# Performance work log

Hardware: AMD Instinct MI355X
Metric: run time of the kernel (lower is better)

Reference implementation:

```python
import jax, jax.numpy as jnp
import numpy as np

# Model dims (MiniCPM-style decode-only LM inside VoxCPM2)
L, B, D = 16, 4, 1024
H, HD, KVH = 16, 64, 8          # query heads, head dim, KV heads (GQA)
DFF = 4096
S = 2048                         # current KV cache length
SCALE_DEPTH = 1.4                # mup depth scaling
EPS = 1e-5
THETA = 10000.0
W_STD = 0.02


def setup_inputs() -> dict:
    key = jax.random.key(0)
    ks = jax.random.split(key, 12)
    return {
        "inputs_embeds": jax.random.normal(ks[0], (B, D), jnp.float32),
        "k_cache": jax.random.normal(ks[1], (L, B, KVH, S, HD), jnp.float32),
        "v_cache": jax.random.normal(ks[2], (L, B, KVH, S, HD), jnp.float32),
        "ln1_w": jnp.ones((L, D), jnp.float32),
        "ln2_w": jnp.ones((L, D), jnp.float32),
        "norm_w": jnp.ones((D,), jnp.float32),
        "wq": jax.random.normal(ks[3], (L, D, H * HD), jnp.float32) * W_STD,
        "wk": jax.random.normal(ks[4], (L, D, KVH * HD), jnp.float32) * W_STD,
        "wv": jax.random.normal(ks[5], (L, D, KVH * HD), jnp.float32) * W_STD,
        "wo": jax.random.normal(ks[6], (L, H * HD, D), jnp.float32) * W_STD,
        "w_gate": jax.random.normal(ks[7], (L, D, DFF), jnp.float32) * W_STD,
        "w_up": jax.random.normal(ks[8], (L, D, DFF), jnp.float32) * W_STD,
        "w_down": jax.random.normal(ks[9], (L, DFF, D), jnp.float32) * W_STD,
        "cache_length": S,  # position id of the token being decoded
    }


def _rmsnorm(x, w):
    return x * jax.lax.rsqrt(jnp.mean(x * x, axis=-1, keepdims=True) + EPS) * w


def _rotate_half(x):
    x1, x2 = jnp.split(x, 2, axis=-1)
    return jnp.concatenate((-x2, x1), axis=-1)


def _decode_step(inputs_embeds, k_cache, v_cache, ln1_w, ln2_w, norm_w,
                 wq, wk, wv, wo, w_gate, w_up, w_down, cache_length):
    # RoPE tables for the single decode position
    pos = jnp.asarray(cache_length, jnp.float32)
    inv_freq = 1.0 / (THETA ** (jnp.arange(0, HD, 2, dtype=jnp.float32) / HD))
    freqs = pos * inv_freq                       # [HD/2]
    emb = jnp.concatenate((freqs, freqs))        # [HD]
    cos, sin = jnp.cos(emb), jnp.sin(emb)

    mup = SCALE_DEPTH / np.sqrt(L)
    scale = 1.0 / np.sqrt(HD)
    G = H // KVH  # query heads per KV head

    def layer(h, ws):
        l1, l2, Wq, Wk, Wv, Wo, Wg, Wu, Wd, kc, vc = ws
        x = _rmsnorm(h, l1)                                  # [B, D]
        q = (x @ Wq).reshape(B, H, HD)
        k = (x @ Wk).reshape(B, KVH, HD)
        v = (x @ Wv).reshape(B, KVH, HD)
        q = q * cos + _rotate_half(q) * sin
        k = k * cos + _rotate_half(k) * sin
        nk = jnp.concatenate((kc, k[:, :, None, :]), axis=2)  # [B, KVH, S+1, HD]
        nv = jnp.concatenate((vc, v[:, :, None, :]), axis=2)
        qg = q.reshape(B, KVH, G, HD)                         # GQA grouping
        scores = jnp.einsum('bkgd,bksd->bkgs', qg, nk) * scale
        p = jax.nn.softmax(scores, axis=-1)
        o = jnp.einsum('bkgs,bksd->bkgd', p, nv).reshape(B, H * HD)
        h = h + (o @ Wo) * mup                                # mup residual
        x = _rmsnorm(h, l2)
        mlp = (jax.nn.silu(x @ Wg) * (x @ Wu)) @ Wd           # SwiGLU
        h = h + mlp * mup
        return h, (nk, nv)

    h, (next_k, next_v) = jax.lax.scan(
        layer, inputs_embeds,
        (ln1_w, ln2_w, wq, wk, wv, wo, w_gate, w_up, w_down, k_cache, v_cache))
    h = _rmsnorm(h, norm_w)
    return h, next_k, next_v


def reference(inputs_embeds, k_cache, v_cache, ln1_w, ln2_w, norm_w,
              wq, wk, wv, wo, w_gate, w_up, w_down, cache_length):
    h, nk, nv = _decode_step(inputs_embeds, k_cache, v_cache, ln1_w, ln2_w,
                             norm_w, wq, wk, wv, wo, w_gate, w_up, w_down,
                             cache_length)
    return h, nk, nv, jnp.asarray(cache_length + 1, jnp.int64)
```

## Files before the change

kernel.cpp:

```cpp
#include <hip/hip_runtime.h>
#include <math.h>

#define MUP 0.35f
#define SCALE 0.125f
#define EPS 1e-5f

#define WS_HA    0
#define WS_HB    4096
#define WS_YMLP  8192
#define WS_YO    12288
#define WS_QKVP  16384
#define WS_OPART 278528
#define WS_GUP   413696

#define OUT_NK  4096
#define OUT_NV  (4096 + 16*4*8*2049*64)
#define OUT_SC  (4096 + 2*16*4*8*2049*64)

__device__ __forceinline__ float wsum64(float v) {
    v += __shfl_xor(v, 32); v += __shfl_xor(v, 16); v += __shfl_xor(v, 8);
    v += __shfl_xor(v, 4);  v += __shfl_xor(v, 2);  v += __shfl_xor(v, 1);
    return v;
}

__device__ __forceinline__ void fma4(float4& a, float s, const float4 w) {
    a.x = fmaf(s, w.x, a.x); a.y = fmaf(s, w.y, a.y);
    a.z = fmaf(s, w.z, a.z); a.w = fmaf(s, w.w, a.w);
}

__global__ __launch_bounds__(256) void k_init(const float* __restrict__ emb,
                                              const int* __restrict__ cl,
                                              float* __restrict__ ws,
                                              float* __restrict__ out) {
    int tid = threadIdx.x;
    float4* ws4 = (float4*)ws;
    float4 z = {0.f, 0.f, 0.f, 0.f};
    if (blockIdx.x == 0) {
        const float4* e4 = (const float4*)emb;
        #pragma unroll
        for (int k = 0; k < 4; ++k) ws4[(WS_HA >> 2) + k * 256 + tid] = e4[k * 256 + tid];
        if (tid == 0) out[OUT_SC] = (float)(cl[0] + 1);
    } else if (blockIdx.x == 1) {
        #pragma unroll
        for (int k = 0; k < 4; ++k) ws4[(WS_YMLP >> 2) + k * 256 + tid] = z;
    } else {
        #pragma unroll
        for (int k = 0; k < 4; ++k) ws4[(WS_YO >> 2) + k * 256 + tid] = z;
    }
}

__global__ __launch_bounds__(512) void k_a(const float* __restrict__ ln1,
                                           const float* __restrict__ wq,
                                           const float* __restrict__ wk,
                                           const float* __restrict__ wv,
                                           float* __restrict__ ws, int l) {
    float4* ws4 = (float4*)ws;
    const int tid = threadIdx.x, w = tid >> 6, lane = tid & 63;
    if (blockIdx.x >= 64) {
        float4 z = {0,0,0,0};
        ws4[(WS_YO >> 2) + (blockIdx.x - 64) * 512 + tid] = z;
        return;
    }
    __shared__ float xs[4][128];
    __shared__ float4 red[8][64][4];
    __shared__ float sred[8][4];
    const int s = blockIdx.x >> 3, xt = blockIdx.x & 7;
    const int t2 = tid & 255;

    float4 hn[4]; float ss[4];
    #pragma unroll
    for (int b = 0; b < 4; ++b) {
        float4 h = ws4[(WS_HA >> 2) + b * 256 + t2];
        float4 y = ws4[(WS_YMLP >> 2) + b * 256 + t2];
        h.x = fmaf(MUP, y.x, h.x); h.y = fmaf(MUP, y.y, h.y);
        h.z = fmaf(MUP, y.z, h.z); h.w = fmaf(MUP, y.w, h.w);
        hn[b] = h;
        ss[b] = h.x*h.x + h.y*h.y + h.z*h.z + h.w*h.w;
    }
    #pragma unroll
    for (int b = 0; b < 4; ++b) {
        float v = wsum64(ss[b]);
        if (lane == 0) sred[w][b] = v;
    }
    __syncthreads();
    float rstd[4];
    #pragma unroll
    for (int b = 0; b < 4; ++b) {
        float tot = 0.f;
        #pragma unroll
        for (int ww = 0; ww < 8; ++ww) tot += sred[ww][b];
        rstd[b] = rsqrtf(tot * (1.f/2048.f) + EPS);
    }
    if (blockIdx.x == 0 && tid < 256) {
        #pragma unroll
        for (int b = 0; b < 4; ++b) ws4[(WS_HB >> 2) + b * 256 + t2] = hn[b];
    }
    {
        int tl = t2 - s * 32;
        if (tl >= 0 && tl < 32) {
            float4 g4 = ((const float4*)ln1)[l * 256 + t2];
            #pragma unroll
            for (int b = 0; b < 4; ++b) {
                float4 xv;
                xv.x = hn[b].x * rstd[b] * g4.x; xv.y = hn[b].y * rstd[b] * g4.y;
                xv.z = hn[b].z * rstd[b] * g4.z; xv.w = hn[b].w * rstd[b] * g4.w;
                ((float4*)xs[b])[tl] = xv;
            }
        }
    }
    __syncthreads();

    const float* Wp; int nc, c;
    if (xt < 4)      { Wp = wq + (size_t)l * 1024 * 1024; nc = 1024; c = xt * 256 + lane * 4; }
    else if (xt < 6) { Wp = wk + (size_t)l * 1024 * 512;  nc = 512;  c = (xt - 4) * 256 + lane * 4; }
    else             { Wp = wv + (size_t)l * 1024 * 512;  nc = 512;  c = (xt - 6) * 256 + lane * 4; }
    const float4* W4 = (const float4*)(Wp + c);
    const size_t nc4 = (size_t)(nc >> 2);
    float4 a0 = {0,0,0,0}, a1 = a0, a2 = a0, a3 = a0;
    #pragma unroll
    for (int ch = 0; ch < 2; ++ch) {
        float4 wr[8];
        #pragma unroll
        for (int i = 0; i < 8; ++i)
            wr[i] = W4[(size_t)(s * 128 + w * 16 + ch * 8 + i) * nc4];
        #pragma unroll
        for (int i = 0; i < 8; ++i) {
            int r = w * 16 + ch * 8 + i;
            fma4(a0, xs[0][r], wr[i]); fma4(a1, xs[1][r], wr[i]);
            fma4(a2, xs[2][r], wr[i]); fma4(a3, xs[3][r], wr[i]);
        }
    }
    red[w][lane][0] = a0; red[w][lane][1] = a1;
    red[w][lane][2] = a2; red[w][lane][3] = a3;
    __syncthreads();
    if (w == 0) {
        float4* QKVP4 = ws4 + (WS_QKVP >> 2);
        #pragma unroll
        for (int b = 0; b < 4; ++b) {
            float4 sv = red[0][lane][b];
            #pragma unroll
            for (int ww = 1; ww < 8; ++ww) {
                float4 t = red[ww][lane][b];
                sv.x += t.x; sv.y += t.y; sv.z += t.z; sv.w += t.w;
            }
            QKVP4[(size_t)(s * 4 + b) * 512 + xt * 64 + lane] = sv;
        }
    }
}

__global__ __launch_bounds__(256) void k_b(const float* __restrict__ kc,
                                           const float* __restrict__ vc,
                                           const int* __restrict__ cl,
                                           float* __restrict__ ws,
                                           float* __restrict__ nk,
                                           float* __restrict__ nv, int l) {
    const int bid = blockIdx.x;
    const int b = bid >> 6, kvh = (bid >> 3) & 7, c = bid & 7;
    const int s0 = c * 256;
    const int tid = threadIdx.x, w = tid >> 6, lane = tid & 63;
    const int sub = lane >> 4, j = lane & 15;
    float4* ws4 = (float4*)ws;
    const float4* QKVP4 = (const float4*)ws4 + (WS_QKVP >> 2);

    __shared__ float4 oac[2][16][16];
    __shared__ float mlm[2][16], mll[2][16];

    const float pos = (float)cl[0];
    float cs4[4], sn4[4];
    #pragma unroll
    for (int m = 0; m < 4; ++m) {
        float t = (float)(4 * (j & 7) + m);
        float fr = pos * __expf(-t * 0.2878231366242557f);
        cs4[m] = cosf(fr); sn4[m] = sinf(fr);
    }
    const float sgn = (j < 8) ? -1.f : 1.f;

    float4 q0 = {0,0,0,0}, q1 = {0,0,0,0};
    #pragma unroll
    for (int sp = 0; sp < 8; ++sp) {
        const float4* qp = QKVP4 + (size_t)(sp * 4 + b) * 512 + kvh * 32;
        float4 t0 = qp[j], t1 = qp[16 + j];
        q0.x += t0.x; q0.y += t0.y; q0.z += t0.z; q0.w += t0.w;
        q1.x += t1.x; q1.y += t1.y; q1.z += t1.z; q1.w += t1.w;
    }
    {
        float4 q0p, q1p;
        q0p.x = __shfl_xor(q0.x, 8); q0p.y = __shfl_xor(q0.y, 8);
        q0p.z = __shfl_xor(q0.z, 8); q0p.w = __shfl_xor(q0.w, 8);
        q1p.x = __shfl_xor(q1.x, 8); q1p.y = __shfl_xor(q1.y, 8);
        q1p.z = __shfl_xor(q1.z, 8); q1p.w = __shfl_xor(q1.w, 8);
        q0.x = q0.x * cs4[0] + sgn * q0p.x * sn4[0];
        q0.y = q0.y * cs4[1] + sgn * q0p.y * sn4[1];
        q0.z = q0.z * cs4[2] + sgn * q0p.z * sn4[2];
        q0.w = q0.w * cs4[3] + sgn * q0p.w * sn4[3];
        q1.x = q1.x * cs4[0] + sgn * q1p.x * sn4[0];
        q1.y = q1.y * cs4[1] + sgn * q1p.y * sn4[1];
        q1.z = q1.z * cs4[2] + sgn * q1p.z * sn4[2];
        q1.w = q1.w * cs4[3] + sgn * q1p.w * sn4[3];
    }

    const size_t cbase = (size_t)((l * 4 + b) * 8 + kvh);
    const float4* kc4 = (const float4*)kc + cbase * 2048 * 16;
    const float4* vc4 = (const float4*)vc + cbase * 2048 * 16;
    float4* nk4 = (float4*)nk + cbase * 2049 * 16;
    float4* nv4 = (float4*)nv + cbase * 2049 * 16;

    float m0 = -1e30f, m1 = -1e30f, l0 = 0.f, l1 = 0.f;
    float4 o0 = {0,0,0,0}, o1 = {0,0,0,0};
    for (int g = 0; g < 4; ++g) {
        const int rb = s0 + g * 64 + w * 16;
        float4 kr[4], vr[4];
        #pragma unroll
        for (int ii = 0; ii < 4; ++ii) {
            int r = rb + ii * 4 + sub;
            kr[ii] = kc4[(size_t)r * 16 + j];
            vr[ii] = vc4[(size_t)r * 16 + j];
        }
        #pragma unroll
        for (int ii = 0; ii < 4; ++ii) {
            int r = rb + ii * 4 + sub;
            nk4[(size_t)r * 16 + j] = kr[ii];
            nv4[(size_t)r * 16 + j] = vr[ii];
        }
        #pragma unroll
        for (int ii = 0; ii < 4; ++ii) {
            float4 kv = kr[ii];
            float d0 = kv.x*q0.x + kv.y*q0.y + kv.z*q0.z + kv.w*q0.w;
            float d1 = kv.x*q1.x + kv.y*q1.y + kv.z*q1.z + kv.w*q1.w;
            d0 += __shfl_xor(d0, 1); d0 += __shfl_xor(d0, 2);
            d0 += __shfl_xor(d0, 4); d0 += __shfl_xor(d0, 8);
            d1 += __shfl_xor(d1, 1); d1 += __shfl_xor(d1, 2);
            d1 += __shfl_xor(d1, 4); d1 += __shfl_xor(d1, 8);
            d0 *= SCALE; d1 *= SCALE;
            float mn0 = fmaxf(m0, d0);
            float e0 = __expf(m0 - mn0), p0 = __expf(d0 - mn0);
            o0.x = o0.x*e0 + p0*kv.x*0.f + p0*vr[ii].x;
            o0.x = fmaf(p0, vr[ii].x, o0.x - p0*vr[ii].x + (o0.x*e0 - o0.x));
            o0 = o0;
            o0.x = 0.f;
            break;
        }
        break;
    }
    m0 = -1e30f; m1 = -1e30f; l0 = 0.f; l1 = 0.f;
    o0 = make_float4(0.f, 0.f, 0.f, 0.f); o1 = make_float4(0.f, 0.f, 0.f, 0.f);
    for (int g = 0; g < 4; ++g) {
        const int rb = s0 + g * 64 + w * 16;
        float4 kr[4], vr[4];
        #pragma unroll
        for (int ii = 0; ii < 4; ++ii) {
            int r = rb + ii * 4 + sub;
            kr[ii] = kc4[(size_t)r * 16 + j];
            vr[ii] = vc4[(size_t)r * 16 + j];
        }
        #pragma unroll
        for (int ii = 0; ii < 4; ++ii) {
            int r = rb + ii * 4 + sub;
            nk4[(size_t)r * 16 + j] = kr[ii];
            nv4[(size_t)r * 16 + j] = vr[ii];
        }
        #pragma unroll
        for (int ii = 0; ii < 4; ++ii) {
            float4 kv = kr[ii];
            float d0 = kv.x*q0.x + kv.y*q0.y + kv.z*q0.z + kv.w*q0.w;
            float d1 = kv.x*q1.x + kv.y*q1.y + kv.z*q1.z + kv.w*q1.w;
            d0 += __shfl_xor(d0, 1); d0 += __shfl_xor(d0, 2);
            d0 += __shfl_xor(d0, 4); d0 += __shfl_xor(d0, 8);
            d1 += __shfl_xor(d1, 1); d1 += __shfl_xor(d1, 2);
            d1 += __shfl_xor(d1, 4); d1 += __shfl_xor(d1, 8);
            d0 *= SCALE; d1 *= SCALE;
            float mn0 = fmaxf(m0, d0);
            float e0 = __expf(m0 - mn0), p0 = __expf(d0 - mn0);
            o0.x = o0.x*e0 + p0*vr[ii].x; o0.y = o0.y*e0 + p0*vr[ii].y;
            o0.z = o0.z*e0 + p0*vr[ii].z; o0.w = o0.w*e0 + p0*vr[ii].w;
            l0 = l0*e0 + p0; m0 = mn0;
            float mn1 = fmaxf(m1, d1);
            float e1 = __expf(m1 - mn1), p1 = __expf(d1 - mn1);
            o1.x = o1.x*e1 + p1*vr[ii].x; o1.y = o1.y*e1 + p1*vr[ii].y;
            o1.z = o1.z*e1 + p1*vr[ii].z; o1.w = o1.w*e1 + p1*vr[ii].w;
            l1 = l1*e1 + p1; m1 = mn1;
        }
    }
    if (c == 7 && w == 0 && sub == 0) {
        float4 kv = {0,0,0,0}, vnew = {0,0,0,0};
        #pragma unroll
        for (int sp = 0; sp < 8; ++sp) {
            const float4* pp = QKVP4 + (size_t)(sp * 4 + b) * 512;
            float4 t0 = pp[256 + kvh * 16 + j];
            float4 t1 = pp[384 + kvh * 16 + j];
            kv.x += t0.x; kv.y += t0.y; kv.z += t0.z; kv.w += t0.w;
            vnew.x += t1.x; vnew.y += t1.y; vnew.z += t1.z; vnew.w += t1.w;
        }
        float4 kp;
        kp.x = __shfl_xor(kv.x, 8); kp.y = __shfl_xor(kv.y, 8);
        kp.z = __shfl_xor(kv.z, 8); kp.w = __shfl_xor(kv.w, 8);
        kv.x = kv.x * cs4[0] + sgn * kp.x * sn4[0];
        kv.y = kv.y * cs4[1] + sgn * kp.y * sn4[1];
        kv.z = kv.z * cs4[2] + sgn * kp.z * sn4[2];
        kv.w = kv.w * cs4[3] + sgn * kp.w * sn4[3];
        nk4[(size_t)2048 * 16 + j] = kv;
        nv4[(size_t)2048 * 16 + j] = vnew;
        float d0 = kv.x*q0.x + kv.y*q0.y + kv.z*q0.z + kv.w*q0.w;
        float d1 = kv.x*q1.x + kv.y*q1.y + kv.z*q1.z + kv.w*q1.w;
        d0 += __shfl_xor(d0, 1); d0 += __shfl_xor(d0, 2);
        d0 += __shfl_xor(d0, 4); d0 += __shfl_xor(d0, 8);
        d1 += __shfl_xor(d1, 1); d1 += __shfl_xor(d1, 2);
        d1 += __shfl_xor(d1, 4); d1 += __shfl_xor(d1, 8);
        d0 *= SCALE; d1 *= SCALE;
        float mn0 = fmaxf(m0, d0);
        float e0 = __expf(m0 - mn0), p0 = __expf(d0 - mn0);
        o0.x = o0.x*e0 + p0*vnew.x; o0.y = o0.y*e0 + p0*vnew.y;
        o0.z = o0.z*e0 + p0*vnew.z; o0.w = o0.w*e0 + p0*vnew.w;
        l0 = l0*e0 + p0; m0 = mn0;
        float mn1 = fmaxf(m1, d1);
        float e1 = __expf(m1 - mn1), p1 = __expf(d1 - mn1);
        o1.x = o1.x*e1 + p1*vnew.x; o1.y = o1.y*e1 + p1*vnew.y;
        o1.z = o1.z*e1 + p1*vnew.z; o1.w = o1.w*e1 + p1*vnew.w;
        l1 = l1*e1 + p1; m1 = mn1;
    }
    const int grp = w * 4 + sub;
    oac[0][grp][j] = o0;
    oac[1][grp][j] = o1;
    if (j == 0) {
        mlm[0][grp] = m0; mll[0][grp] = l0;
        mlm[1][grp] = m1; mll[1][grp] = l1;
    }
    __syncthreads();
    if (tid < 128) {
        const int h = tid >> 6, d = tid & 63;
        const float* oa = (const float*)&oac[h][0][0];
        float M = -1e30f;
        #pragma unroll
        for (int g2 = 0; g2 < 16; ++g2) M = fmaxf(M, mlm[h][g2]);
        float ot = 0.f, lt = 0.f;
        #pragma unroll
        for (int g2 = 0; g2 < 16; ++g2) {
            float e = __expf(mlm[h][g2] - M);
            ot += oa[g2 * 64 + d] * e;
            lt += mll[h][g2] * e;
        }
        int pbase = WS_OPART + ((b * 8 + kvh) * 8 + c) * 132;
        ws[pbase + h * 64 + d] = ot;
        if (d == 0) { ws[pbase + 128 + 2 * h] = M; ws[pbase + 129 + 2 * h] = lt; }
    }
}

__global__ __launch_bounds__(512) void k_c(const float* __restrict__ wo,
                                           float* __restrict__ ws, int l) {
    float4* ws4 = (float4*)ws;
    const int tid = threadIdx.x, w = tid >> 6, lane = tid & 63;
    if (blockIdx.x >= 32) {
        float4 z = {0,0,0,0};
        ws4[(WS_YMLP >> 2) + (blockIdx.x - 32) * 512 + tid] = z;
        return;
    }
    __shared__ float xs[4][128];
    __shared__ float4 red[8][64][4];
    const int xt = blockIdx.x & 3, s = blockIdx.x >> 2;
    {
        const int bb = tid >> 7, rr = tid & 127;
        const int r = s * 128 + rr;
        const int kvh = r >> 7, g = (r >> 6) & 1, d = r & 63;
        const float* bp = ws + WS_OPART + (size_t)((bb * 8 + kvh) * 8) * 132;
        float m = -1e30f;
        #pragma unroll
        for (int cc = 0; cc < 8; ++cc)
            m = fmaxf(m, bp[cc * 132 + 128 + 2 * g]);
        float lt = 0.f, ot = 0.f;
        #pragma unroll
        for (int cc = 0; cc < 8; ++cc) {
            float f = __expf(bp[cc * 132 + 128 + 2 * g] - m);
            lt += bp[cc * 132 + 129 + 2 * g] * f;
            ot += bp[cc * 132 + g * 64 + d] * f;
        }
        xs[bb][rr] = ot / lt;
    }
    __syncthreads();
    const float4* W4 = (const float4*)(wo + (size_t)l * 1024 * 1024 + xt * 256 + lane * 4);
    float4 a0 = {0,0,0,0}, a1 = a0, a2 = a0, a3 = a0;
    #pragma unroll
    for (int ch = 0; ch < 2; ++ch) {
        float4 wr[8];
        #pragma unroll
        for (int i = 0; i < 8; ++i)
            wr[i] = W4[(size_t)(s * 128 + w * 16 + ch * 8 + i) * 256];
        #pragma unroll
        for (int i = 0; i < 8; ++i) {
            int r = w * 16 + ch * 8 + i;
            fma4(a0, xs[0][r], wr[i]); fma4(a1, xs[1][r], wr[i]);
            fma4(a2, xs[2][r], wr[i]); fma4(a3, xs[3][r], wr[i]);
        }
    }
    red[w][lane][0] = a0; red[w][lane][1] = a1;
    red[w][lane][2] = a2; red[w][lane][3] = a3;
    __syncthreads();
    if (w == 0) {
        int c = xt * 256 + lane * 4;
        #pragma unroll
        for (int b = 0; b < 4; ++b) {
            float4 sv = red[0][lane][b];
            #pragma unroll
            for (int ww = 1; ww < 8; ++ww) {
                float4 t = red[ww][lane][b];
                sv.x += t.x; sv.y += t.y; sv.z += t.z; sv.w += t.w;
            }
            atomicAdd(&ws[WS_YO + b * 1024 + c + 0], sv.x);
            atomicAdd(&ws[WS_YO + b * 1024 + c + 1], sv.y);
            atomicAdd(&ws[WS_YO + b * 1024 + c + 2], sv.z);
            atomicAdd(&ws[WS_YO + b * 1024 + c + 3], sv.w);
        }
    }
}

__global__ __launch_bounds__(512) void k_d(const float* __restrict__ ln2,
                                           const float* __restrict__ wg,
                                           const float* __restrict__ wu,
                                           float* __restrict__ ws, int l) {
    float4* ws4 = (float4*)ws;
    const int tid = threadIdx.x, w = tid >> 6, lane = tid & 63;
    __shared__ float xs[4][128];
    __shared__ float4 red[8][64][4];
    __shared__ float sred[8][4];
    const int t16 = blockIdx.x, y = blockIdx.y;
    const int t2 = tid & 255;

    float4 hn[4]; float ss[4];
    #pragma unroll
    for (int b = 0; b < 4; ++b) {
        float4 h = ws4[(WS_HB >> 2) + b * 256 + t2];
        float4 yv = ws4[(WS_YO >> 2) + b * 256 + t2];
        h.x = fmaf(MUP, yv.x, h.x); h.y = fmaf(MUP, yv.y, h.y);
        h.z = fmaf(MUP, yv.z, h.z); h.w = fmaf(MUP, yv.w, h.w);
        hn[b] = h;
        ss[b] = h.x*h.x + h.y*h.y + h.z*h.z + h.w*h.w;
    }
    #pragma unroll
    for (int b = 0; b < 4; ++b) {
        float v = wsum64(ss[b]);
        if (lane == 0) sred[w][b] = v;
    }
    __syncthreads();
    float rstd[4];
    #pragma unroll
    for (int b = 0; b < 4; ++b) {
        float tot = 0.f;
        #pragma unroll
        for (int ww = 0; ww < 8; ++ww) tot += sred[ww][b];
        rstd[b] = rsqrtf(tot * (1.f/2048.f) + EPS);
    }
    if (blockIdx.x == 0 && blockIdx.y == 0 && tid < 256) {
        #pragma unroll
        for (int b = 0; b < 4; ++b) ws4[(WS_HA >> 2) + b * 256 + t2] = hn[b];
    }
    {
        int tl = t2 - y * 32;
        if (tl >= 0 && tl < 32) {
            float4 g4 = ((const float4*)ln2)[l * 256 + t2];
            #pragma unroll
            for (int b = 0; b < 4; ++b) {
                float4 xv;
                xv.x = hn[b].x * rstd[b] * g4.x; xv.y = hn[b].y * rstd[b] * g4.y;
                xv.z = hn[b].z * rstd[b] * g4.z; xv.w = hn[b].w * rstd[b] * g4.w;
                ((float4*)xs[b])[tl] = xv;
            }
        }
    }
    __syncthreads();
    float4* GUP4 = ws4 + (WS_GUP >> 2);

    #pragma unroll
    for (int mat = 0; mat < 2; ++mat) {
        const float* Wm = (mat ? wu : wg) + (size_t)l * 1024 * 4096;
        const float4* W4 = (const float4*)(Wm + t16 * 256 + lane * 4);
        float4 a0 = {0,0,0,0}, a1 = a0, a2 = a0, a3 = a0;
        #pragma unroll
        for (int ch = 0; ch < 2; ++ch) {
            float4 wr[8];
            #pragma unroll
            for (int i = 0; i < 8; ++i)
                wr[i] = W4[(size_t)(y * 128 + w * 16 + ch * 8 + i) * 1024];
            #pragma unroll
            for (int i = 0; i < 8; ++i) {
                int r = w * 16 + ch * 8 + i;
                fma4(a0, xs[0][r], wr[i]); fma4(a1, xs[1][r], wr[i]);
                fma4(a2, xs[2][r], wr[i]); fma4(a3, xs[3][r], wr[i]);
            }
        }
        red[w][lane][0] = a0; red[w][lane][1] = a1;
        red[w][lane][2] = a2; red[w][lane][3] = a3;
        __syncthreads();
        if (w == 0) {
            #pragma unroll
            for (int b = 0; b < 4; ++b) {
                float4 sv = red[0][lane][b];
                #pragma unroll
                for (int ww = 1; ww < 8; ++ww) {
                    float4 t = red[ww][lane][b];
                    sv.x += t.x; sv.y += t.y; sv.z += t.z; sv.w += t.w;
                }
                GUP4[(size_t)((mat * 8 + y) * 4 + b) * 1024 + t16 * 64 + lane] = sv;
            }
        }
        __syncthreads();
    }
}

__global__ __launch_bounds__(512) void k_e(const float* __restrict__ wd,
                                           float* __restrict__ ws, int l) {
    float4* ws4 = (float4*)ws;
    const int tid = threadIdx.x, w = tid >> 6, lane = tid & 63;
    __shared__ float ts[4][128];
    __shared__ float4 red[8][64][4];
    const int xt = blockIdx.x, s = blockIdx.y;
    if (tid < 128) {
        const int bb = tid >> 5, i = tid & 31;
        const int f4 = s * 32 + i;
        const float4* GUP4 = (const float4*)ws4 + (WS_GUP >> 2);
        float4 g = {0,0,0,0}, u = {0,0,0,0};
        #pragma unroll
        for (int sp = 0; sp < 8; ++sp) {
            float4 gv = GUP4[(size_t)(sp * 4 + bb) * 1024 + f4];
            float4 uv = GUP4[(size_t)((8 + sp) * 4 + bb) * 1024 + f4];
            g.x += gv.x; g.y += gv.y; g.z += gv.z; g.w += gv.w;
            u.x += uv.x; u.y += uv.y; u.z += uv.z; u.w += uv.w;
        }
        float4 t;
        t.x = (g.x / (1.f + __expf(-g.x))) * u.x;
        t.y = (g.y / (1.f + __expf(-g.y))) * u.y;
        t.z = (g.z / (1.f + __expf(-g.z))) * u.z;
        t.w = (g.w / (1.f + __expf(-g.w))) * u.w;
        ((float4*)ts[bb])[i] = t;
    }
    __syncthreads();
    const float4* W4 = (const float4*)(wd + (size_t)l * 4096 * 1024 + xt * 256 + lane * 4);
    float4 a0 = {0,0,0,0}, a1 = a0, a2 = a0, a3 = a0;
    #pragma unroll
    for (int ch = 0; ch < 2; ++ch) {
        float4 wr[8];
        #pragma unroll
        for (int i = 0; i < 8; ++i)
            wr[i] = W4[(size_t)(s * 128 + w * 16 + ch * 8 + i) * 256];
        #pragma unroll
        for (int i = 0; i < 8; ++i) {
            int r = w * 16 + ch * 8 + i;
            fma4(a0, ts[0][r], wr[i]); fma4(a1, ts[1][r], wr[i]);
            fma4(a2, ts[2][r], wr[i]); fma4(a3, ts[3][r], wr[i]);
        }
    }
    red[w][lane][0] = a0; red[w][lane][1] = a1;
    red[w][lane][2] = a2; red[w][lane][3] = a3;
    __syncthreads();
    if (w == 0) {
        int c = xt * 256 + lane * 4;
        #pragma unroll
        for (int b = 0; b < 4; ++b) {
            float4 sv = red[0][lane][b];
            #pragma unroll
            for (int ww = 1; ww < 8; ++ww) {
                float4 t = red[ww][lane][b];
                sv.x += t.x; sv.y += t.y; sv.z += t.z; sv.w += t.w;
            }
            atomicAdd(&ws[WS_YMLP + b * 1024 + c + 0], sv.x);
            atomicAdd(&ws[WS_YMLP + b * 1024 + c + 1], sv.y);
            atomicAdd(&ws[WS_YMLP + b * 1024 + c + 2], sv.z);
            atomicAdd(&ws[WS_YMLP + b * 1024 + c + 3], sv.w);
        }
    }
}

__global__ __launch_bounds__(256) void k_final(const float* __restrict__ normw,
                                               float* __restrict__ ws,
                                               float* __restrict__ out) {
    float4* ws4 = (float4*)ws;
    int tid = threadIdx.x;
    int b = blockIdx.x, w = tid >> 6, lane = tid & 63;
    __shared__ float sred[4];
    float4 h = ws4[(WS_HA >> 2) + b * 256 + tid];
    float4 y = ws4[(WS_YMLP >> 2) + b * 256 + tid];
    h.x = fmaf(MUP, y.x, h.x); h.y = fmaf(MUP, y.y, h.y);
    h.z = fmaf(MUP, y.z, h.z); h.w = fmaf(MUP, y.w, h.w);
    float ssv = h.x*h.x + h.y*h.y + h.z*h.z + h.w*h.w;
    float v = wsum64(ssv);
    if (lane == 0) sred[w] = v;
    __syncthreads();
    float rstd = rsqrtf((sred[0] + sred[1] + sred[2] + sred[3]) * (1.f/1024.f) + EPS);
    float4 g4 = ((const float4*)normw)[tid];
    float4 o;
    o.x = h.x * rstd * g4.x; o.y = h.y * rstd * g4.y;
    o.z = h.z * rstd * g4.z; o.w = h.w * rstd * g4.w;
    ((float4*)out)[b * 256 + tid] = o;
}

extern "C" void kernel_launch(void* const* d_in, const int* in_sizes, int n_in,
                              void* d_out, int out_size, void* d_ws, size_t ws_size,
                              hipStream_t stream) {
    const float* emb  = (const float*)d_in[0];
    const float* kc   = (const float*)d_in[1];
    const float* vc   = (const float*)d_in[2];
    const float* ln1  = (const float*)d_in[3];
    const float* ln2  = (const float*)d_in[4];
    const float* nrmw = (const float*)d_in[5];
    const float* wq   = (const float*)d_in[6];
    const float* wk   = (const float*)d_in[7];
    const float* wv   = (const float*)d_in[8];
    const float* wo   = (const float*)d_in[9];
    const float* wg   = (const float*)d_in[10];
    const float* wu   = (const float*)d_in[11];
    const float* wd   = (const float*)d_in[12];
    const int*   cl   = (const int*)d_in[13];

    float* out = (float*)d_out;
    float* ws  = (float*)d_ws;
    float* nk  = out + OUT_NK;
    float* nv  = out + OUT_NV;

    k_init<<<3, 256, 0, stream>>>(emb, cl, ws, out);
    for (int l = 0; l < 16; ++l) {
        k_a<<<66, 512, 0, stream>>>(ln1, wq, wk, wv, ws, l);
        k_b<<<256, 256, 0, stream>>>(kc, vc, cl, ws, nk, nv, l);
        k_c<<<34, 512, 0, stream>>>(wo, ws, l);
        k_d<<<dim3(16, 8), 512, 0, stream>>>(ln2, wg, wu, ws, l);
        k_e<<<dim3(4, 32), 512, 0, stream>>>(wd, ws, l);
    }
    k_final<<<4, 256, 0, stream>>>(nrmw, ws, out);
}
```

Before: 904.5 us.

## Double-buffer KV cache loads, use nontemporal stores, drop dead warm-up loop

Removes a leftover warm-up loop that loaded and stored a KV chunk and then broke out, which duplicated cache traffic. The main attention loop now prefetches the next 64-row K/V chunk into a second register buffer while the current chunk is processed. The copies into the new cache use nontemporal stores so streaming writes do not pollute the cache. Register pressure rises because of the doubled kr/vr buffers, which could reduce occupancy.

New measurement: 887.5 us (median of 2 runs). About the same (-1.9%).

```diff
diff --git a/kernel.cpp b/kernel.cpp
--- a/kernel.cpp
+++ b/kernel.cpp
@@ -4,6 +4,8 @@
 #define MUP 0.35f
 #define SCALE 0.125f
 #define EPS 1e-5f
+
+typedef float f32x4 __attribute__((ext_vector_type(4)));
 
 #define WS_HA    0
 #define WS_HB    4096
@@ -26,6 +28,11 @@
 __device__ __forceinline__ void fma4(float4& a, float s, const float4 w) {
     a.x = fmaf(s, w.x, a.x); a.y = fmaf(s, w.y, a.y);
     a.z = fmaf(s, w.z, a.z); a.w = fmaf(s, w.w, a.w);
+}
+
+__device__ __forceinline__ void nt_store4(const float4 v, float4* p) {
+    f32x4 t = {v.x, v.y, v.z, v.w};
+    __builtin_nontemporal_store(t, (f32x4*)p);
 }
 
 __global__ __launch_bounds__(256) void k_init(const float* __restrict__ emb,
@@ -207,24 +214,36 @@
 
     float m0 = -1e30f, m1 = -1e30f, l0 = 0.f, l1 = 0.f;
     float4 o0 = {0,0,0,0}, o1 = {0,0,0,0};
+    float4 kr[2][4], vr[2][4];
+
+    #pragma unroll
+    for (int ii = 0; ii < 4; ++ii) {
+        int r = s0 + w * 16 + ii * 4 + sub;
+        kr[0][ii] = kc4[(size_t)r * 16 + j];
+        vr[0][ii] = vc4[(size_t)r * 16 + j];
+    }
+    #pragma unroll
     for (int g = 0; g < 4; ++g) {
+        const int cur = g & 1, nxt = cur ^ 1;
         const int rb = s0 + g * 64 + w * 16;
-        float4 kr[4], vr[4];
+        if (g < 3) {
+            const int rn = s0 + (g + 1) * 64 + w * 16;
+            #pragma unroll
+            for (int ii = 0; ii < 4; ++ii) {
+                int r = rn + ii * 4 + sub;
+                kr[nxt][ii] = kc4[(size_t)r * 16 + j];
+                vr[nxt][ii] = vc4[(size_t)r * 16 + j];
+            }
+        }
         #pragma unroll
         for (int ii = 0; ii < 4; ++ii) {
             int r = rb + ii * 4 + sub;
-            kr[ii] = kc4[(size_t)r * 16 + j];
-            vr[ii] = vc4[(size_t)r * 16 + j];
+            nt_store4(kr[cur][ii], &nk4[(size_t)r * 16 + j]);
+            nt_store4(vr[cur][ii], &nv4[(size_t)r * 16 + j]);
         }
         #pragma unroll
         for (int ii = 0; ii < 4; ++ii) {
-            int r = rb + ii * 4 + sub;
-            nk4[(size_t)r * 16 + j] = kr[ii];
-            nv4[(size_t)r * 16 + j] = vr[ii];
-        }
-        #pragma unroll
-        for (int ii = 0; ii < 4; ++ii) {
-            float4 kv = kr[ii];
+            float4 kv = kr[cur][ii];
             float d0 = kv.x*q0.x + kv.y*q0.y + kv.z*q0.z + kv.w*q0.w;
             float d1 = kv.x*q1.x + kv.y*q1.y + kv.z*q1.z + kv.w*q1.w;
             d0 += __shfl_xor(d0, 1); d0 += __shfl_xor(d0, 2);
@@ -234,50 +253,13 @@
             d0 *= SCALE; d1 *= SCALE;
             float mn0 = fmaxf(m0, d0);
             float e0 = __expf(m0 - mn0), p0 = __expf(d0 - mn0);
-            o0.x = o0.x*e0 + p0*kv.x*0.f + p0*vr[ii].x;
-            o0.x = fmaf(p0, vr[ii].x, o0.x - p0*vr[ii].x + (o0.x*e0 - o0.x));
-            o0 = o0;
-            o0.x = 0.f;
-            break;
-        }
-        break;
-    }
-    m0 = -1e30f; m1 = -1e30f; l0 = 0.f; l1 = 0.f;
-    o0 = make_float4(0.f, 0.f, 0.f, 0.f); o1 = make_float4(0.f, 0.f, 0.f, 0.f);
-    for (int g = 0; g < 4; ++g) {
-        const int rb = s0 + g * 64 + w * 16;
-        float4 kr[4], vr[4];
-        #pragma unroll
-        for (int ii = 0; ii < 4; ++ii) {
-            int r = rb + ii * 4 + sub;
-            kr[ii] = kc4[(size_t)r * 16 + j];
-            vr[ii] = vc4[(size_t)r * 16 + j];
-        }
-        #pragma unroll
-        for (int ii = 0; ii < 4; ++ii) {
-            int r = rb + ii * 4 + sub;
-            nk4[(size_t)r * 16 + j] = kr[ii];
-            nv4[(size_t)r * 16 + j] = vr[ii];
-        }
-        #pragma unroll
-        for (int ii = 0; ii < 4; ++ii) {
-            float4 kv = kr[ii];
-            float d0 = kv.x*q0.x + kv.y*q0.y + kv.z*q0.z + kv.w*q0.w;
-            float d1 = kv.x*q1.x + kv.y*q1.y + kv.z*q1.z + kv.w*q1.w;
-            d0 += __shfl_xor(d0, 1); d0 += __shfl_xor(d0, 2);
-            d0 += __shfl_xor(d0, 4); d0 += __shfl_xor(d0, 8);
-            d1 += __shfl_xor(d1, 1); d1 += __shfl_xor(d1, 2);
-            d1 += __shfl_xor(d1, 4); d1 += __shfl_xor(d1, 8);
-            d0 *= SCALE; d1 *= SCALE;
-            float mn0 = fmaxf(m0, d0);
-            float e0 = __expf(m0 - mn0), p0 = __expf(d0 - mn0);
-            o0.x = o0.x*e0 + p0*vr[ii].x; o0.y = o0.y*e0 + p0*vr[ii].y;
-            o0.z = o0.z*e0 + p0*vr[ii].z; o0.w = o0.w*e0 + p0*vr[ii].w;
+            o0.x = o0.x*e0 + p0*vr[cur][ii].x; o0.y = o0.y*e0 + p0*vr[cur][ii].y;
+            o0.z = o0.z*e0 + p0*vr[cur][ii].z; o0.w = o0.w*e0 + p0*vr[cur][ii].w;
             l0 = l0*e0 + p0; m0 = mn0;
             float mn1 = fmaxf(m1, d1);
             float e1 = __expf(m1 - mn1), p1 = __expf(d1 - mn1);
-            o1.x = o1.x*e1 + p1*vr[ii].x; o1.y = o1.y*e1 + p1*vr[ii].y;
-            o1.z = o1.z*e1 + p1*vr[ii].z; o1.w = o1.w*e1 + p1*vr[ii].w;
+            o1.x = o1.x*e1 + p1*vr[cur][ii].x; o1.y = o1.y*e1 + p1*vr[cur][ii].y;
+            o1.z = o1.z*e1 + p1*vr[cur][ii].z; o1.w = o1.w*e1 + p1*vr[cur][ii].w;
             l1 = l1*e1 + p1; m1 = mn1;
         }
     }
```
